# Performance work log

Measured on AMD Instinct MI355X. Metric: run time of the kernel, lower is better.

## Reference

```python
import jax, jax.numpy as jnp
import numpy as np


def quantize_uniform(x, n_bits, clip):
    # clamp to [-clip, clip], round to 2^(1-n_bits)*clip grid, cap at clip*(1-b)
    b = 2.0 ** (1 - n_bits)
    xc = jnp.clip(x, -clip, clip)
    return clip * jnp.minimum(b * jnp.round(xc / (b * clip)), 1.0 - b)


def quantize_act(x, n_bits, clip):
    # clip to [0, clip], round to 2^-n_bits grid, cap at 1 - 2^-n_bits
    s = 2.0 ** n_bits
    xc = jnp.clip(x, 0.0, clip)
    return jnp.minimum(jnp.round(xc * s) / s, 1.0 - 1.0 / s)


def qconv(x, w, b, pad):
    # fake-quantized conv: weights/bias quant(8,1), input quant(8,4), output quant(8,8)
    wq = quantize_uniform(w, 8, 1.0)
    bq = quantize_uniform(b, 8, 1.0)
    xq = quantize_uniform(x, 8, 4.0)
    y = jax.lax.conv_general_dilated(
        xq, wq, window_strides=(1, 1), padding=[(pad, pad), (pad, pad)],
        dimension_numbers=('NCHW', 'OIHW', 'NCHW'))
    y = y + bq[None, :, None, None]
    return quantize_uniform(y, 8, 8.0)


def setup_inputs() -> dict:
    key = jax.random.key(0)
    ks = jax.random.split(key, 7)
    N, Cin, H, W = 32, 128, 56, 56
    Sq, E1, E3 = 32, 128, 128
    x = jax.random.normal(ks[0], (N, Cin, H, W), dtype=jnp.float32)
    w_sq = jax.random.normal(ks[1], (Sq, Cin, 1, 1), dtype=jnp.float32) * 0.05
    b_sq = jax.random.normal(ks[2], (Sq,), dtype=jnp.float32) * 0.05
    w_e1 = jax.random.normal(ks[3], (E1, Sq, 1, 1), dtype=jnp.float32) * 0.05
    b_e1 = jax.random.normal(ks[4], (E1,), dtype=jnp.float32) * 0.05
    w_e3 = jax.random.normal(ks[5], (E3, Sq, 3, 3), dtype=jnp.float32) * 0.05
    b_e3 = jax.random.normal(ks[6], (E3,), dtype=jnp.float32) * 0.05
    return {'x': x, 'w_sq': w_sq, 'b_sq': b_sq, 'w_e1': w_e1, 'b_e1': b_e1,
            'w_e3': w_e3, 'b_e3': b_e3}


def reference(x, w_sq, b_sq, w_e1, b_e1, w_e3, b_e3):
    h = jax.nn.relu(qconv(x, w_sq, b_sq, pad=0))
    h = quantize_act(h, 13, 4.0)
    y1 = jax.nn.relu(qconv(h, w_e1, b_e1, pad=0))
    y3 = jax.nn.relu(qconv(h, w_e3, b_e3, pad=1))
    return jnp.concatenate([y1, y3], axis=1)
```

## Files before the change

kernel.cpp:

```cpp
#include <hip/hip_runtime.h>
#include <stdint.h>

typedef __bf16 bf16x8 __attribute__((ext_vector_type(8)));
typedef float  f32x4  __attribute__((ext_vector_type(4)));

#define HW   3136
#define WID  56
#define CIN  128
#define SQ   32

#define OFF_BSQ 0
#define OFF_BE  32
#define WSQF_BYTES_OFF 1152
#define WE1F_BYTES_OFF 9344
#define WE3F_BYTES_OFF 17536

__device__ __forceinline__ float quant_w8(float x){
  float xc = fminf(fmaxf(x,-1.f),1.f);
  return fminf(rintf(xc*128.f)*0.0078125f, 0.9921875f);
}
__device__ __forceinline__ ushort wq_int_bf16(float x){
  float xc = fminf(fmaxf(x,-1.f),1.f);
  float n = fminf(rintf(xc*128.f), 127.f);
  return (ushort)(__float_as_uint(n)>>16);
}
__device__ __forceinline__ uint pack2f(float a, float b){
  return (__float_as_uint(a)>>16) | (__float_as_uint(b)&0xffff0000u);
}

__global__ void prep_kernel(const float* __restrict__ wsq, const float* __restrict__ bsq,
                            const float* __restrict__ we1, const float* __restrict__ be1,
                            const float* __restrict__ we3, const float* __restrict__ be3,
                            float* __restrict__ ws){
  int tid = blockIdx.x*blockDim.x+threadIdx.x;
  int nth = gridDim.x*blockDim.x;
  ushort* wsqf = (ushort*)((char*)ws + WSQF_BYTES_OFF);
  ushort* we1f = (ushort*)((char*)ws + WE1F_BYTES_OFF);
  ushort* we3f = (ushort*)((char*)ws + WE3F_BYTES_OFF);
  for (int i=tid;i<SQ;i+=nth) ws[OFF_BSQ+i]=quant_w8(bsq[i]);
  for (int i=tid;i<256;i+=nth) ws[OFF_BE+i] = (i<128)? quant_w8(be1[i]) : quant_w8(be3[i-128]);
  for (int i=tid;i<4096;i+=nth){
    int mfkc=i>>9, l=(i>>3)&63, j=i&7;
    int mf=mfkc>>2, kc=mfkc&3;
    int co=mf*16+(l&15), ci=kc*32+(l>>4)*8+j;
    wsqf[i] = wq_int_bf16(wsq[co*CIN+ci]);
  }
  for (int i=tid;i<4096;i+=nth){
    int mf=i>>9, l=(i>>3)&63, j=i&7;
    int co=mf*16+(l&15), ci=(l>>4)*8+j;
    we1f[i] = wq_int_bf16(we1[co*SQ+ci]);
  }
  for (int i=tid;i<36864;i+=nth){
    int mf=i/4608, r=i-mf*4608, t=r>>9, l=(r>>3)&63, j=r&7;
    int co=mf*16+(l&15), ci=(l>>4)*8+j;
    we3f[i] = wq_int_bf16(we3[(co*SQ+ci)*9+t]);
  }
}

#define LOADX(dst, b) { \
  int px_ = base_px + (b)*16 + colg; \
  int pxc_ = (px_ < limit) ? px_ : (limit-1); \
  const float* xp_ = xb + pxc_; \
  _Pragma("unroll") \
  for (int kc_=0;kc_<4;++kc_) \
    _Pragma("unroll") \
    for (int j_=0;j_<8;++j_) \
      dst[kc_*8+j_] = xp_[(size_t)(kc_*32 + kg*8 + j_)*HW]; }

#define PROCX(src, b) { \
  bf16x8 Bf_[4]; \
  _Pragma("unroll") \
  for (int kc_=0;kc_<4;++kc_){ \
    float m_[8]; \
    _Pragma("unroll") \
    for (int j_=0;j_<8;++j_){ \
      float v_ = fminf(fmaxf(src[kc_*8+j_],-4.f),4.f); \
      m_[j_] = fminf(rintf(v_*32.f), 127.f); \
    } \
    union { uint u[4]; bf16x8 v; } cv_; \
    _Pragma("unroll") \
    for (int q_=0;q_<4;++q_) cv_.u[q_] = pack2f(m_[q_*2], m_[q_*2+1]); \
    Bf_[kc_] = cv_.v; \
  } \
  f32x4 a0_ = (f32x4){0.f,0.f,0.f,0.f}; \
  f32x4 a1_ = (f32x4){0.f,0.f,0.f,0.f}; \
  _Pragma("unroll") \
  for (int kc_=0;kc_<4;++kc_){ \
    a0_ = __builtin_amdgcn_mfma_f32_16x16x32_bf16(W[kc_],   Bf_[kc_], a0_, 0,0,0); \
    a1_ = __builtin_amdgcn_mfma_f32_16x16x32_bf16(W[4+kc_], Bf_[kc_], a1_, 0,0,0); \
  } \
  int px_ = base_px + (b)*16 + colg; \
  if (px_ < limit){ \
    int rr_ = px_/WID, c_ = px_ - rr_*WID; \
    int ph_ = (rr_ - R0 + 1)*58 + c_ + 1; \
    _Pragma("unroll") \
    for (int mf_=0;mf_<2;++mf_){ \
      f32x4 a_ = mf_ ? a1_ : a0_; \
      float m_[4]; \
      _Pragma("unroll") \
      for (int r_=0;r_<4;++r_){ \
        float y_ = fmaf(a_[r_], 0.000244140625f, bias[mf_][r_]); \
        y_ = fminf(fmaxf(y_,-8.f),8.f); \
        y_ = fminf(rintf(y_*16.f)*0.0625f, 7.9375f); \
        y_ = fmaxf(y_,0.f); \
        y_ = fminf(y_,4.f); \
        y_ = fminf(y_,0.9998779296875f); \
        m_[r_] = rintf(y_*32.f); \
      } \
      int chunk_ = mf_*2 + (kg>>1); \
      int idx_ = ph_*4 + (chunk_ ^ ((ph_>>1)&3)); \
      uint* dst_ = (uint*)&lds4[idx_] + (kg&1)*2; \
      dst_[0] = pack2f(m_[0], m_[1]); \
      dst_[1] = pack2f(m_[2], m_[3]); \
    } \
  } }

__global__ __launch_bounds__(256, 2) void fire_kernel(const float* __restrict__ x,
    const float* __restrict__ ws, float* __restrict__ out){
  __shared__ uint4 lds4[1392];
  int bry = blockIdx.x;
  int n   = blockIdx.y;
  int tid = threadIdx.x, w = tid>>6, lane = tid&63;
  int colg = lane&15, kg = lane>>4;
  int R0 = bry*4;
  int vr0 = (R0==0) ? 0 : R0-1;
  int vr1 = (R0+4 > 55) ? 55 : R0+4;
  int limit = (vr1+1)*WID;
  int nblk = ((vr1-vr0+1)*WID + 15)>>4;
  int base_px = vr0*WID;

  uint4 z = make_uint4(0,0,0,0);
  for (int i=tid; i<1392; i+=256) lds4[i] = z;
  __syncthreads();

  {
    const bf16x8* wsqf = (const bf16x8*)((const char*)ws + WSQF_BYTES_OFF);
    bf16x8 W[8];
    #pragma unroll
    for (int q=0;q<8;++q) W[q] = wsqf[q*64 + lane];
    float bias[2][4];
    #pragma unroll
    for (int mf=0;mf<2;++mf)
      #pragma unroll
      for (int r=0;r<4;++r) bias[mf][r] = ws[OFF_BSQ + mf*16 + kg*4 + r];

    const float* xb = x + (size_t)n*CIN*HW;
    float xvA[32], xvB[32];
    int b = w;
    if (b < nblk){
      LOADX(xvA, b);
      while (true){
        int b2 = b + 4;
        if (b2 < nblk){
          LOADX(xvB, b2);
          PROCX(xvA, b);
          int b3 = b2 + 4;
          if (b3 < nblk){
            LOADX(xvA, b3);
            PROCX(xvB, b2);
            b = b3;
          } else { PROCX(xvB, b2); break; }
        } else { PROCX(xvA, b); break; }
      }
    }
  }
  __syncthreads();

  int wid = w;
  const bf16x8* we1f = (const bf16x8*)((const char*)ws + WE1F_BYTES_OFF);
  const bf16x8* we3f = (const bf16x8*)((const char*)ws + WE3F_BYTES_OFF);
  const bf16x8* lbase = (const bf16x8*)lds4;

  float biasv[4];
  #pragma unroll
  for (int mi=0;mi<4;++mi) biasv[mi] = ws[OFF_BE + (wid+mi*4)*16 + colg];

  #pragma unroll
  for (int s=0; s<2; ++s){
    int baseh[7];
    #pragma unroll
    for (int nf=0;nf<7;++nf){
      int p = s*112 + nf*16 + colg;
      int rr = p/WID, c = p - rr*WID;
      baseh[nf] = (rr+1)*58 + c + 1;
    }

    f32x4 acc[4][7];
    #pragma unroll
    for (int mi=0;mi<4;++mi)
      #pragma unroll
      for (int nf=0;nf<7;++nf)
        acc[mi][nf] = (f32x4){0.f,0.f,0.f,0.f};

    #pragma unroll
    for (int t=0;t<9;++t){
      int off = (t/3 - 1)*58 + (t%3 - 1);
      bf16x8 B[7];
      #pragma unroll
      for (int nf=0;nf<7;++nf){
        int ph = baseh[nf] + off;
        int idx = ph*4 + (kg ^ ((ph>>1)&3));
        B[nf] = lbase[idx];
      }
      bf16x8 A2 = we3f[(wid*9+t)*64 + lane];
      bf16x8 A3 = we3f[((wid+4)*9+t)*64 + lane];
      #pragma unroll
      for (int nf=0;nf<7;++nf){
        acc[2][nf] = __builtin_amdgcn_mfma_f32_16x16x32_bf16(B[nf], A2, acc[2][nf], 0,0,0);
        acc[3][nf] = __builtin_amdgcn_mfma_f32_16x16x32_bf16(B[nf], A3, acc[3][nf], 0,0,0);
      }
      if (t==4){
        bf16x8 A0 = we1f[wid*64 + lane];
        bf16x8 A1 = we1f[(wid+4)*64 + lane];
        #pragma unroll
        for (int nf=0;nf<7;++nf){
          acc[0][nf] = __builtin_amdgcn_mfma_f32_16x16x32_bf16(B[nf], A0, acc[0][nf], 0,0,0);
          acc[1][nf] = __builtin_amdgcn_mfma_f32_16x16x32_bf16(B[nf], A1, acc[1][nf], 0,0,0);
        }
      }
    }

    #pragma unroll
    for (int mi=0;mi<4;++mi){
      int co = (wid+mi*4)*16 + colg;
      float* opb = out + (size_t)(n*256+co)*HW + R0*WID + s*112 + kg*4;
      #pragma unroll
      for (int nf=0;nf<7;++nf){
        f32x4 a = acc[mi][nf];
        f32x4 yv;
        #pragma unroll
        for (int r=0;r<4;++r){
          float y = fmaf(a[r], 0.000244140625f, biasv[mi]);
          y = fminf(fmaxf(y,-8.f),8.f);
          y = fminf(rintf(y*16.f)*0.0625f, 7.9375f);
          y = fmaxf(y,0.f);
          yv[r] = y;
        }
        *(f32x4*)(opb + nf*16) = yv;
      }
    }
  }
}

extern "C" void kernel_launch(void* const* d_in, const int* in_sizes, int n_in,
                              void* d_out, int out_size, void* d_ws, size_t ws_size,
                              hipStream_t stream){
  const float* x   = (const float*)d_in[0];
  const float* wsq = (const float*)d_in[1];
  const float* bsq = (const float*)d_in[2];
  const float* we1 = (const float*)d_in[3];
  const float* be1 = (const float*)d_in[4];
  const float* we3 = (const float*)d_in[5];
  const float* be3 = (const float*)d_in[6];
  float* out = (float*)d_out;
  float* ws  = (float*)d_ws;

  hipLaunchKernelGGL(prep_kernel, dim3(64), dim3(256), 0, stream,
                     wsq, bsq, we1, be1, we3, be3, ws);
  hipLaunchKernelGGL(fire_kernel, dim3(14, 32), dim3(256), 0, stream, x, ws, out);
}
```

Before: 44.99 us.

## Double row tile per block and overlap squeeze loads with expand convolution

Each block now covers 8 output rows with 512 threads instead of 4 rows with 256. That halves the redundant halo recomputation of the squeeze layer. The expand phase is split into four 2-row passes, and the squeeze input for later rows is loaded and processed inside those passes, so global loads overlap with expand MFMA work. Each wave now owns a single output-channel group for both the 1x1 and 3x3 expand, and the squeeze weights are reloaded per tile rather than held in registers. The grid shrinks to 224 blocks, fewer than the number of CUs, which risks leaving compute units idle.

```diff
diff --git a/kernel.cpp b/kernel.cpp
--- a/kernel.cpp
+++ b/kernel.cpp
@@ -57,17 +57,21 @@
   }
 }
 
-#define LOADX(dst, b) { \
-  int px_ = base_px + (b)*16 + colg; \
-  int pxc_ = (px_ < limit) ? px_ : (limit-1); \
-  const float* xp_ = xb + pxc_; \
+#define LOADX(dst, bl) { \
+  int g_ = gbase + (bl)*16 + colg; \
+  int gc_ = g_ < 0 ? 0 : (g_ > HW-1 ? HW-1 : g_); \
+  const float* xp_ = xb + gc_; \
   _Pragma("unroll") \
   for (int kc_=0;kc_<4;++kc_) \
     _Pragma("unroll") \
     for (int j_=0;j_<8;++j_) \
       dst[kc_*8+j_] = xp_[(size_t)(kc_*32 + kg*8 + j_)*HW]; }
 
-#define PROCX(src, b) { \
+#define PROCX(src, bl) { \
+  const bf16x8* wsqf_ = (const bf16x8*)((const char*)ws + WSQF_BYTES_OFF); \
+  bf16x8 W_[8]; \
+  _Pragma("unroll") \
+  for (int q_=0;q_<8;++q_) W_[q_] = wsqf_[q_*64 + lane]; \
   bf16x8 Bf_[4]; \
   _Pragma("unroll") \
   for (int kc_=0;kc_<4;++kc_){ \
@@ -86,159 +90,139 @@
   f32x4 a1_ = (f32x4){0.f,0.f,0.f,0.f}; \
   _Pragma("unroll") \
   for (int kc_=0;kc_<4;++kc_){ \
-    a0_ = __builtin_amdgcn_mfma_f32_16x16x32_bf16(W[kc_],   Bf_[kc_], a0_, 0,0,0); \
-    a1_ = __builtin_amdgcn_mfma_f32_16x16x32_bf16(W[4+kc_], Bf_[kc_], a1_, 0,0,0); \
+    a0_ = __builtin_amdgcn_mfma_f32_16x16x32_bf16(W_[kc_],   Bf_[kc_], a0_, 0,0,0); \
+    a1_ = __builtin_amdgcn_mfma_f32_16x16x32_bf16(W_[4+kc_], Bf_[kc_], a1_, 0,0,0); \
   } \
-  int px_ = base_px + (b)*16 + colg; \
-  if (px_ < limit){ \
-    int rr_ = px_/WID, c_ = px_ - rr_*WID; \
-    int ph_ = (rr_ - R0 + 1)*58 + c_ + 1; \
-    _Pragma("unroll") \
-    for (int mf_=0;mf_<2;++mf_){ \
-      f32x4 a_ = mf_ ? a1_ : a0_; \
-      float m_[4]; \
-      _Pragma("unroll") \
-      for (int r_=0;r_<4;++r_){ \
-        float y_ = fmaf(a_[r_], 0.000244140625f, bias[mf_][r_]); \
-        y_ = fminf(fmaxf(y_,-8.f),8.f); \
-        y_ = fminf(rintf(y_*16.f)*0.0625f, 7.9375f); \
-        y_ = fmaxf(y_,0.f); \
-        y_ = fminf(y_,4.f); \
-        y_ = fminf(y_,0.9998779296875f); \
-        m_[r_] = rintf(y_*32.f); \
-      } \
-      int chunk_ = mf_*2 + (kg>>1); \
-      int idx_ = ph_*4 + (chunk_ ^ ((ph_>>1)&3)); \
-      uint* dst_ = (uint*)&lds4[idx_] + (kg&1)*2; \
-      dst_[0] = pack2f(m_[0], m_[1]); \
-      dst_[1] = pack2f(m_[2], m_[3]); \
+  int lp_ = (bl)*16 + colg; \
+  int g_  = gbase + lp_; \
+  int lr_ = lp_/WID, c_ = lp_ - lr_*WID; \
+  int ph_ = lr_*58 + c_ + 1; \
+  bool valid_ = (g_ >= 0) && (g_ < HW); \
+  _Pragma("unroll") \
+  for (int mf_=0;mf_<2;++mf_){ \
+    f32x4 a_ = mf_ ? a1_ : a0_; \
+    float m_[4]; \
+    _Pragma("unroll") \
+    for (int r_=0;r_<4;++r_){ \
+      float y_ = fmaf(a_[r_], 0.000244140625f, bias[mf_][r_]); \
+      y_ = fminf(fmaxf(y_,-8.f),8.f); \
+      y_ = fminf(rintf(y_*16.f)*0.0625f, 7.9375f); \
+      y_ = fmaxf(y_,0.f); \
+      y_ = fminf(y_,4.f); \
+      y_ = fminf(y_,0.9998779296875f); \
+      m_[r_] = valid_ ? rintf(y_*32.f) : 0.f; \
     } \
+    int chunk_ = mf_*2 + (kg>>1); \
+    int idx_ = ph_*4 + (chunk_ ^ ((ph_>>1)&3)); \
+    uint* dst_ = (uint*)&lds4[idx_] + (kg&1)*2; \
+    dst_[0] = pack2f(m_[0], m_[1]); \
+    dst_[1] = pack2f(m_[2], m_[3]); \
   } }
 
-__global__ __launch_bounds__(256, 2) void fire_kernel(const float* __restrict__ x,
+__global__ __launch_bounds__(512) void fire_kernel(const float* __restrict__ x,
     const float* __restrict__ ws, float* __restrict__ out){
-  __shared__ uint4 lds4[1392];
+  __shared__ uint4 lds4[2320];
   int bry = blockIdx.x;
   int n   = blockIdx.y;
   int tid = threadIdx.x, w = tid>>6, lane = tid&63;
   int colg = lane&15, kg = lane>>4;
-  int R0 = bry*4;
-  int vr0 = (R0==0) ? 0 : R0-1;
-  int vr1 = (R0+4 > 55) ? 55 : R0+4;
-  int limit = (vr1+1)*WID;
-  int nblk = ((vr1-vr0+1)*WID + 15)>>4;
-  int base_px = vr0*WID;
+  int R0 = bry*8;
+  int gbase = (R0-1)*WID;
+  const float* xb = x + (size_t)n*CIN*HW;
+
+  float bias[2][4];
+  #pragma unroll
+  for (int mf=0;mf<2;++mf)
+    #pragma unroll
+    for (int r=0;r<4;++r) bias[mf][r] = ws[OFF_BSQ + mf*16 + kg*4 + r];
 
   uint4 z = make_uint4(0,0,0,0);
-  for (int i=tid; i<1392; i+=256) lds4[i] = z;
+  for (int i=tid; i<2320; i+=512) lds4[i] = z;
   __syncthreads();
 
-  {
-    const bf16x8* wsqf = (const bf16x8*)((const char*)ws + WSQF_BYTES_OFF);
-    bf16x8 W[8];
-    #pragma unroll
-    for (int q=0;q<8;++q) W[q] = wsqf[q*64 + lane];
-    float bias[2][4];
-    #pragma unroll
-    for (int mf=0;mf<2;++mf)
-      #pragma unroll
-      for (int r=0;r<4;++r) bias[mf][r] = ws[OFF_BSQ + mf*16 + kg*4 + r];
-
-    const float* xb = x + (size_t)n*CIN*HW;
-    float xvA[32], xvB[32];
-    int b = w;
-    if (b < nblk){
-      LOADX(xvA, b);
-      while (true){
-        int b2 = b + 4;
-        if (b2 < nblk){
-          LOADX(xvB, b2);
-          PROCX(xvA, b);
-          int b3 = b2 + 4;
-          if (b3 < nblk){
-            LOADX(xvA, b3);
-            PROCX(xvB, b2);
-            b = b3;
-          } else { PROCX(xvB, b2); break; }
-        } else { PROCX(xvA, b); break; }
-      }
-    }
-  }
+  float xv[32];
+  LOADX(xv, w);      PROCX(xv, w);
+  LOADX(xv, w+8);    PROCX(xv, w+8);
   __syncthreads();
 
-  int wid = w;
   const bf16x8* we1f = (const bf16x8*)((const char*)ws + WE1F_BYTES_OFF);
   const bf16x8* we3f = (const bf16x8*)((const char*)ws + WE3F_BYTES_OFF);
   const bf16x8* lbase = (const bf16x8*)lds4;
-
-  float biasv[4];
-  #pragma unroll
-  for (int mi=0;mi<4;++mi) biasv[mi] = ws[OFF_BE + (wid+mi*4)*16 + colg];
-
-  #pragma unroll
-  for (int s=0; s<2; ++s){
+  float be1v = ws[OFF_BE + w*16 + colg];
+  float be3v = ws[OFF_BE + 128 + w*16 + colg];
+
+  for (int i=0;i<4;++i){
+    bool doProc = (i<2) || (i==2 && w<3);
+    int nb = (i<2) ? (16 + i*8 + w) : (32 + w);
+    if (doProc) LOADX(xv, nb);
+
     int baseh[7];
     #pragma unroll
     for (int nf=0;nf<7;++nf){
-      int p = s*112 + nf*16 + colg;
+      int p = i*112 + nf*16 + colg;
       int rr = p/WID, c = p - rr*WID;
       baseh[nf] = (rr+1)*58 + c + 1;
     }
 
-    f32x4 acc[4][7];
-    #pragma unroll
-    for (int mi=0;mi<4;++mi)
-      #pragma unroll
-      for (int nf=0;nf<7;++nf)
-        acc[mi][nf] = (f32x4){0.f,0.f,0.f,0.f};
-
-    #pragma unroll
-    for (int t=0;t<9;++t){
-      int off = (t/3 - 1)*58 + (t%3 - 1);
-      bf16x8 B[7];
+    {
+      bf16x8 A0 = we1f[w*64 + lane];
+      f32x4 acc1[7];
       #pragma unroll
       for (int nf=0;nf<7;++nf){
-        int ph = baseh[nf] + off;
+        int ph = baseh[nf];
         int idx = ph*4 + (kg ^ ((ph>>1)&3));
-        B[nf] = lbase[idx];
-      }
-      bf16x8 A2 = we3f[(wid*9+t)*64 + lane];
-      bf16x8 A3 = we3f[((wid+4)*9+t)*64 + lane];
+        acc1[nf] = __builtin_amdgcn_mfma_f32_16x16x32_bf16(lbase[idx], A0,
+                     (f32x4){0.f,0.f,0.f,0.f}, 0,0,0);
+      }
+      int co = w*16 + colg;
+      float* op = out + (size_t)(n*256+co)*HW + R0*WID + i*112 + kg*4;
       #pragma unroll
       for (int nf=0;nf<7;++nf){
-        acc[2][nf] = __builtin_amdgcn_mfma_f32_16x16x32_bf16(B[nf], A2, acc[2][nf], 0,0,0);
-        acc[3][nf] = __builtin_amdgcn_mfma_f32_16x16x32_bf16(B[nf], A3, acc[3][nf], 0,0,0);
-      }
-      if (t==4){
-        bf16x8 A0 = we1f[wid*64 + lane];
-        bf16x8 A1 = we1f[(wid+4)*64 + lane];
+        f32x4 a = acc1[nf], yv;
+        #pragma unroll
+        for (int r=0;r<4;++r){
+          float y = fmaf(a[r], 0.000244140625f, be1v);
+          y = fminf(fmaxf(y,-8.f),8.f);
+          y = fminf(rintf(y*16.f)*0.0625f, 7.9375f);
+          yv[r] = fmaxf(y,0.f);
+        }
+        *(f32x4*)(op + nf*16) = yv;
+      }
+    }
+
+    {
+      f32x4 acc[7];
+      #pragma unroll
+      for (int nf=0;nf<7;++nf) acc[nf] = (f32x4){0.f,0.f,0.f,0.f};
+      #pragma unroll
+      for (int t=0;t<9;++t){
+        int off = (t/3 - 1)*58 + (t%3 - 1);
+        bf16x8 A = we3f[(w*9+t)*64 + lane];
         #pragma unroll
         for (int nf=0;nf<7;++nf){
-          acc[0][nf] = __builtin_amdgcn_mfma_f32_16x16x32_bf16(B[nf], A0, acc[0][nf], 0,0,0);
-          acc[1][nf] = __builtin_amdgcn_mfma_f32_16x16x32_bf16(B[nf], A1, acc[1][nf], 0,0,0);
+          int ph = baseh[nf] + off;
+          int idx = ph*4 + (kg ^ ((ph>>1)&3));
+          acc[nf] = __builtin_amdgcn_mfma_f32_16x16x32_bf16(lbase[idx], A, acc[nf], 0,0,0);
         }
       }
-    }
-
-    #pragma unroll
-    for (int mi=0;mi<4;++mi){
-      int co = (wid+mi*4)*16 + colg;
-      float* opb = out + (size_t)(n*256+co)*HW + R0*WID + s*112 + kg*4;
+      int co = w*16 + colg;
+      float* op = out + (size_t)(n*256+128+co)*HW + R0*WID + i*112 + kg*4;
       #pragma unroll
       for (int nf=0;nf<7;++nf){
-        f32x4 a = acc[mi][nf];
-        f32x4 yv;
+        f32x4 a = acc[nf], yv;
         #pragma unroll
         for (int r=0;r<4;++r){
-          float y = fmaf(a[r], 0.000244140625f, biasv[mi]);
+          float y = fmaf(a[r], 0.000244140625f, be3v);
           y = fminf(fmaxf(y,-8.f),8.f);
           y = fminf(rintf(y*16.f)*0.0625f, 7.9375f);
-          y = fmaxf(y,0.f);
-          yv[r] = y;
+          yv[r] = fmaxf(y,0.f);
         }
-        *(f32x4*)(opb + nf*16) = yv;
+        *(f32x4*)(op + nf*16) = yv;
       }
     }
+
+    if (doProc) PROCX(xv, nb);
+    if (i<3) __syncthreads();
   }
 }
 
@@ -257,5 +241,5 @@
 
   hipLaunchKernelGGL(prep_kernel, dim3(64), dim3(256), 0, stream,
                      wsq, bsq, we1, be1, we3, be3, ws);
-  hipLaunchKernelGGL(fire_kernel, dim3(14, 32), dim3(256), 0, stream, x, ws, out);
-}
+  hipLaunchKernelGGL(fire_kernel, dim3(7, 32), dim3(512), 0, stream, x, ws, out);
+}
```

After: 48.51 us. +7.8%, slower.
